# Optimization experiments

Measured on AMD Instinct MI355X. Metric: run time of the kernel, lower is better.

Reference implementation:

```python
import jax, jax.numpy as jnp
import numpy as np

N, E = 100000, 1600000
IN_C, HID_C, OUT_C = 128, 64, 40


def setup_inputs() -> dict:
    key = jax.random.key(0)
    ks = jax.random.split(key, 8)
    s = lambda fan_in: 1.0 / np.sqrt(fan_in)
    return {
        "x": jax.random.normal(ks[0], (N, IN_C), dtype=jnp.float32),
        "edge_index": jax.random.randint(ks[1], (2, E), 0, N, dtype=jnp.int64),
        # SAGEConv layer 1: lin_l (on aggregated neighbors, with bias) + lin_r (root, no bias)
        "W_l1": jax.random.uniform(ks[2], (IN_C, HID_C), jnp.float32, -s(IN_C), s(IN_C)),
        "b_l1": jnp.zeros((HID_C,), jnp.float32),
        "W_r1": jax.random.uniform(ks[3], (IN_C, HID_C), jnp.float32, -s(IN_C), s(IN_C)),
        # SAGEConv layer 2
        "W_l2": jax.random.uniform(ks[4], (HID_C, OUT_C), jnp.float32, -s(HID_C), s(HID_C)),
        "b_l2": jnp.zeros((OUT_C,), jnp.float32),
        "W_r2": jax.random.uniform(ks[5], (HID_C, OUT_C), jnp.float32, -s(HID_C), s(HID_C)),
    }


def _sage_conv(x, src, dst, W_l, b_l, W_r, n_nodes):
    # mean-aggregate neighbor features: scatter-add x[src] onto dst, divide by degree
    agg = jax.ops.segment_sum(x[src], dst, num_segments=n_nodes)  # [N, F]
    deg = jax.ops.segment_sum(jnp.ones((src.shape[0],), x.dtype), dst, num_segments=n_nodes)
    mean = agg / jnp.maximum(deg, 1.0)[:, None]
    return mean @ W_l + b_l + x @ W_r


def reference(x, edge_index, W_l1, b_l1, W_r1, W_l2, b_l2, W_r2):
    src, dst = edge_index[0], edge_index[1]  # messages flow src -> dst
    # eval mode: dropout is identity
    hid = _sage_conv(x, src, dst, W_l1, b_l1, W_r1, N)
    hid = jax.nn.relu(hid)
    out = _sage_conv(hid, src, dst, W_l2, b_l2, W_r2, N)
    return jax.nn.log_softmax(out, axis=1)
```

## Files before the change

### kernel.cpp

```cpp
#include <hip/hip_runtime.h>
#include <hip/hip_bf16.h>

#define N_NODES 100000
#define E_EDGES 1600000
#define IN_C 128
#define HID_C 64
#define OUT_C 40

#define NBUCK 196
#define BCAP 9216
#define B1_EPT 16
#define B1_CHUNK (256 * B1_EPT)
#define B1_GRID ((E_EDGES + B1_CHUNK - 1) / B1_CHUNK)

typedef unsigned short ushort_t;
typedef unsigned int uint_t;
typedef unsigned char uchar_t;
typedef __attribute__((ext_vector_type(8))) short bf16x8;
typedef __attribute__((ext_vector_type(4))) float f32x4;
typedef __attribute__((ext_vector_type(2))) float f32x2;

__device__ __forceinline__ float bfu2f(ushort_t u) {
    return __uint_as_float(((uint_t)u) << 16);
}
__device__ __forceinline__ ushort_t f2bfu(float f) {
    uint_t u = __float_as_uint(f);
    return (ushort_t)((u + 0x7FFFu + ((u >> 16) & 1u)) >> 16);
}
__device__ __forceinline__ uchar_t f2fp8(float f) {
    int p = __builtin_amdgcn_cvt_pk_fp8_f32(f, f, 0, false);
    return (uchar_t)(p & 0xff);
}
__device__ __forceinline__ float fp8_1(int u) {
    f32x2 f = __builtin_amdgcn_cvt_pk_f32_fp8(u, false);
    return f.x;
}

__global__ __launch_bounds__(256) void k_bucket(const int* __restrict__ src, const int* __restrict__ dst,
                                                int* __restrict__ bcur, int* __restrict__ bucket) {
    __shared__ int cnt[NBUCK];
    __shared__ int base[NBUCK];
    const int t = threadIdx.x;
    const int e0 = blockIdx.x * B1_CHUNK;

    for (int i = t; i < NBUCK; i += 256) cnt[i] = 0;
    __syncthreads();

    int myp[B1_EPT];
    int myb[B1_EPT];
#pragma unroll
    for (int j = 0; j < B1_EPT; ++j) {
        int e = e0 + t + j * 256;
        if (e < E_EDGES) {
            int d = dst[e];
            myp[j] = src[e] | ((d & 511) << 17);
            myb[j] = d >> 9;
            atomicAdd(&cnt[myb[j]], 1);
        } else {
            myb[j] = -1;
        }
    }
    __syncthreads();
    for (int i = t; i < NBUCK; i += 256) {
        base[i] = atomicAdd(&bcur[i], cnt[i]);
        cnt[i] = 0;
    }
    __syncthreads();
#pragma unroll
    for (int j = 0; j < B1_EPT; ++j) {
        if (myb[j] >= 0) {
            int b = myb[j];
            int loc = atomicAdd(&cnt[b], 1);
            int pos = base[b] + loc;
            if (pos < BCAP) bucket[(size_t)b * BCAP + pos] = myp[j];
        }
    }
}

__global__ __launch_bounds__(256) void k_scanS(const int* __restrict__ bcur, int* __restrict__ bbase,
                                               int* __restrict__ rowptr) {
    __shared__ int tmp[256];
    int t = threadIdx.x;
    int v = (t < NBUCK) ? min(bcur[t], BCAP) : 0;
    tmp[t] = v;
    __syncthreads();
    for (int off = 1; off < 256; off <<= 1) {
        int a = (t >= off) ? tmp[t - off] : 0;
        __syncthreads();
        tmp[t] += a;
        __syncthreads();
    }
    if (t < NBUCK) bbase[t] = tmp[t] - v;
    if (t == 0) rowptr[N_NODES] = tmp[255];
}

__global__ __launch_bounds__(256) void k_csr(const int* __restrict__ bucket, const int* __restrict__ bcur,
                                             const int* __restrict__ bbase,
                                             int* __restrict__ rowptr, int* __restrict__ csr) {
    __shared__ int hist[512];
    __shared__ int sc[2][512];
    __shared__ int cur[512];
    __shared__ int csrbuf[BCAP];
    const int t = threadIdx.x;
    const int b = blockIdx.x;
    const int n0 = b << 9;
    const int nb = min(512, N_NODES - n0);
    const int sz = min(bcur[b], BCAP);
    const int cbase = bbase[b];
    const int* bdata = bucket + (size_t)b * BCAP;

    for (int i = t; i < 512; i += 256) hist[i] = 0;
    __syncthreads();
    for (int i = t; i < sz; i += 256) {
        int p = bdata[i];
        atomicAdd(&hist[p >> 17], 1);
    }
    __syncthreads();
    for (int i = t; i < 512; i += 256) sc[0][i] = hist[i];
    __syncthreads();
    int pp = 0;
    for (int off = 1; off < 512; off <<= 1) {
        for (int i = t; i < 512; i += 256)
            sc[1 - pp][i] = sc[pp][i] + ((i >= off) ? sc[pp][i - off] : 0);
        __syncthreads();
        pp ^= 1;
    }
    for (int i = t; i < 512; i += 256) {
        int exc = sc[pp][i] - hist[i];
        cur[i] = exc;
        if (i < nb) rowptr[n0 + i] = cbase + exc;
    }
    __syncthreads();
    for (int i = t; i < sz; i += 256) {
        int p = bdata[i];
        int pos = atomicAdd(&cur[p >> 17], 1);
        csrbuf[pos] = p & 0x1FFFF;
    }
    __syncthreads();
    for (int i = t; i < sz; i += 256)
        csr[cbase + i] = csrbuf[i];
}

__global__ __launch_bounds__(256) void k_wprep(const float* __restrict__ Wl1, const float* __restrict__ Wr1,
                                               const float* __restrict__ Wl2, const float* __restrict__ Wr2,
                                               ushort_t* __restrict__ Wt1, ushort_t* __restrict__ Wt2) {
    int i = blockIdx.x * 256 + threadIdx.x;
    if (i < 128 * 128) {
        int n = i >> 7, k = i & 127;
        float v = (n < 64) ? Wl1[k * 64 + n] : Wr1[k * 64 + (n - 64)];
        Wt1[n * 128 + k] = f2bfu(v);
    }
    if (i < 80 * 64) {
        int n = i >> 6, k = i & 63;
        float v = (n < 40) ? Wl2[k * 40 + n] : Wr2[k * 40 + (n - 40)];
        Wt2[n * 64 + k] = f2bfu(v);
    }
}

__global__ __launch_bounds__(256) void k_gemm1(const float* __restrict__ x,
                                               const ushort_t* __restrict__ Wt,
                                               uchar_t* __restrict__ h1l,
                                               float* __restrict__ h1r) {
    __shared__ ushort_t xs[64 * 136];
    __shared__ ushort_t wsm[128 * 136];
    const int t = threadIdx.x;
    const int row_base = blockIdx.x * 64;

    for (int i = t; i < 128 * 16; i += 256) {
        int n = i >> 4, seg = i & 15;
        uint4 v = *(const uint4*)(Wt + n * 128 + seg * 8);
        *(uint4*)(wsm + n * 136 + seg * 8) = v;
    }
    for (int i = t; i < 64 * 32; i += 256) {
        int row = i >> 5, seg = i & 31;
        int gr = row_base + row;
        float4 v = make_float4(0.f, 0.f, 0.f, 0.f);
        if (gr < N_NODES) v = *(const float4*)(x + (size_t)gr * IN_C + seg * 4);
        ushort4 u;
        u.x = f2bfu(v.x); u.y = f2bfu(v.y); u.z = f2bfu(v.z); u.w = f2bfu(v.w);
        *(ushort4*)(xs + row * 136 + seg * 4) = u;
    }
    __syncthreads();

    const int wv = t >> 6, lane = t & 63;
    const int m = lane & 15, quad = lane >> 4;
    const int m0 = wv * 16;

    bf16x8 a[4];
#pragma unroll
    for (int kk = 0; kk < 4; ++kk)
        a[kk] = *(const bf16x8*)(xs + (m0 + m) * 136 + kk * 32 + quad * 8);

    f32x4 acc[8];
#pragma unroll
    for (int nt = 0; nt < 8; ++nt) acc[nt] = (f32x4){0.f, 0.f, 0.f, 0.f};

#pragma unroll
    for (int nt = 0; nt < 8; ++nt) {
#pragma unroll
        for (int kk = 0; kk < 4; ++kk) {
            bf16x8 b = *(const bf16x8*)(wsm + (nt * 16 + m) * 136 + kk * 32 + quad * 8);
            acc[nt] = __builtin_amdgcn_mfma_f32_16x16x32_bf16(a[kk], b, acc[nt], 0, 0, 0);
        }
    }

    const int grow_base = row_base + m0 + quad * 4;
#pragma unroll
    for (int r = 0; r < 4; ++r) {
        int grow = grow_base + r;
        if (grow < N_NODES) {
#pragma unroll
            for (int nt = 0; nt < 4; ++nt)
                h1l[(size_t)grow * HID_C + nt * 16 + m] = f2fp8(acc[nt][r]);
#pragma unroll
            for (int nt = 4; nt < 8; ++nt)
                h1r[(size_t)grow * HID_C + (nt - 4) * 16 + m] = acc[nt][r];
        }
    }
}

__global__ __launch_bounds__(256) void k_agg1(const int* __restrict__ rowptr, const int* __restrict__ csr,
                                              const uchar_t* __restrict__ h1l, const float* __restrict__ h1r,
                                              const float* __restrict__ b1, ushort_t* __restrict__ hid) {
    int row = (blockIdx.x * 256 + threadIdx.x) >> 6;
    int lane = threadIdx.x & 63;
    if (row >= N_NODES) return;
    int start = rowptr[row];
    int end = rowptr[row + 1];
    const uchar_t* colp = h1l + lane;
    float acc = 0.0f;
    int e = start;
    for (; e + 8 <= end; e += 8) {
        int s0 = csr[e],     s1 = csr[e + 1], s2 = csr[e + 2], s3 = csr[e + 3];
        int s4 = csr[e + 4], s5 = csr[e + 5], s6 = csr[e + 6], s7 = csr[e + 7];
        float v0 = fp8_1(colp[(size_t)s0 << 6]);
        float v1 = fp8_1(colp[(size_t)s1 << 6]);
        float v2 = fp8_1(colp[(size_t)s2 << 6]);
        float v3 = fp8_1(colp[(size_t)s3 << 6]);
        float v4 = fp8_1(colp[(size_t)s4 << 6]);
        float v5 = fp8_1(colp[(size_t)s5 << 6]);
        float v6 = fp8_1(colp[(size_t)s6 << 6]);
        float v7 = fp8_1(colp[(size_t)s7 << 6]);
        acc += ((v0 + v1) + (v2 + v3)) + ((v4 + v5) + (v6 + v7));
    }
    for (; e < end; ++e)
        acc += fp8_1(colp[(size_t)csr[e] << 6]);

    float inv = __builtin_amdgcn_rcpf(fmaxf((float)(end - start), 1.0f));
    float h = fmaxf(acc * inv + h1r[(size_t)row * HID_C + lane] + b1[lane], 0.0f);
    hid[(size_t)row * HID_C + lane] = f2bfu(h);
}

__global__ __launch_bounds__(256) void k_gemm2(const ushort_t* __restrict__ hid,
                                               const ushort_t* __restrict__ Wt,
                                               uchar_t* __restrict__ h2l,
                                               float* __restrict__ h2r) {
    __shared__ ushort_t hs[64 * 72];
    __shared__ ushort_t wsm[80 * 72];
    const int t = threadIdx.x;
    const int row_base = blockIdx.x * 64;

    for (int i = t; i < 80 * 8; i += 256) {
        int n = i >> 3, seg = i & 7;
        uint4 v = *(const uint4*)(Wt + n * 64 + seg * 8);
        *(uint4*)(wsm + n * 72 + seg * 8) = v;
    }
    for (int i = t; i < 64 * 8; i += 256) {
        int row = i >> 3, seg = i & 7;
        int gr = row_base + row;
        uint4 v = make_uint4(0u, 0u, 0u, 0u);
        if (gr < N_NODES) v = *(const uint4*)(hid + (size_t)gr * HID_C + seg * 8);
        *(uint4*)(hs + row * 72 + seg * 8) = v;
    }
    __syncthreads();

    const int wv = t >> 6, lane = t & 63;
    const int m = lane & 15, quad = lane >> 4;
    const int m0 = wv * 16;

    bf16x8 a[2];
#pragma unroll
    for (int kk = 0; kk < 2; ++kk)
        a[kk] = *(const bf16x8*)(hs + (m0 + m) * 72 + kk * 32 + quad * 8);

    f32x4 acc[5];
#pragma unroll
    for (int nt = 0; nt < 5; ++nt) acc[nt] = (f32x4){0.f, 0.f, 0.f, 0.f};

#pragma unroll
    for (int nt = 0; nt < 5; ++nt) {
#pragma unroll
        for (int kk = 0; kk < 2; ++kk) {
            bf16x8 b = *(const bf16x8*)(wsm + (nt * 16 + m) * 72 + kk * 32 + quad * 8);
            acc[nt] = __builtin_amdgcn_mfma_f32_16x16x32_bf16(a[kk], b, acc[nt], 0, 0, 0);
        }
    }

    const int grow_base = row_base + m0 + quad * 4;
#pragma unroll
    for (int r = 0; r < 4; ++r) {
        int grow = grow_base + r;
        if (grow < N_NODES) {
#pragma unroll
            for (int nt = 0; nt < 5; ++nt) {
                int col = nt * 16 + m;
                float v = acc[nt][r];
                if (col < OUT_C) h2l[(size_t)grow * 64 + col] = f2fp8(v);
                else             h2r[(size_t)grow * OUT_C + (col - OUT_C)] = v;
            }
        }
    }
}

__global__ __launch_bounds__(256) void k_agg2(const int* __restrict__ rowptr, const int* __restrict__ csr,
                                              const uchar_t* __restrict__ h2l, const float* __restrict__ h2r,
                                              const float* __restrict__ b2, float* __restrict__ out) {
    int row = (blockIdx.x * 256 + threadIdx.x) >> 6;
    int lane = threadIdx.x & 63;
    if (row >= N_NODES) return;
    int start = rowptr[row];
    int end = rowptr[row + 1];
    const uchar_t* colp = h2l + lane;
    float acc = 0.0f;
    int e = start;
    for (; e + 8 <= end; e += 8) {
        int s0 = csr[e],     s1 = csr[e + 1], s2 = csr[e + 2], s3 = csr[e + 3];
        int s4 = csr[e + 4], s5 = csr[e + 5], s6 = csr[e + 6], s7 = csr[e + 7];
        float v0 = fp8_1(colp[(size_t)s0 << 6]);
        float v1 = fp8_1(colp[(size_t)s1 << 6]);
        float v2 = fp8_1(colp[(size_t)s2 << 6]);
        float v3 = fp8_1(colp[(size_t)s3 << 6]);
        float v4 = fp8_1(colp[(size_t)s4 << 6]);
        float v5 = fp8_1(colp[(size_t)s5 << 6]);
        float v6 = fp8_1(colp[(size_t)s6 << 6]);
        float v7 = fp8_1(colp[(size_t)s7 << 6]);
        acc += ((v0 + v1) + (v2 + v3)) + ((v4 + v5) + (v6 + v7));
    }
    for (; e < end; ++e)
        acc += fp8_1(colp[(size_t)csr[e] << 6]);

    float inv = __builtin_amdgcn_rcpf(fmaxf((float)(end - start), 1.0f));
    float v = -1e30f;
    if (lane < OUT_C)
        v = acc * inv + h2r[(size_t)row * OUT_C + lane] + b2[lane];
    float m = v;
#pragma unroll
    for (int off = 1; off <= 32; off <<= 1)
        m = fmaxf(m, __shfl_xor(m, off));
    float ex = expf(v - m);
    float s = ex;
#pragma unroll
    for (int off = 1; off <= 32; off <<= 1)
        s += __shfl_xor(s, off);
    float res = v - m - logf(s);
    if (lane < OUT_C)
        out[(size_t)row * OUT_C + lane] = res;
}

extern "C" void kernel_launch(void* const* d_in, const int* in_sizes, int n_in,
                              void* d_out, int out_size, void* d_ws, size_t ws_size,
                              hipStream_t stream) {
    const float* x   = (const float*)d_in[0];
    const int*   ei  = (const int*)d_in[1];
    const float* Wl1 = (const float*)d_in[2];
    const float* b1  = (const float*)d_in[3];
    const float* Wr1 = (const float*)d_in[4];
    const float* Wl2 = (const float*)d_in[5];
    const float* b2  = (const float*)d_in[6];
    const float* Wr2 = (const float*)d_in[7];

    size_t u = 0;
    int*      bucket = (int*)d_ws;             u += (size_t)NBUCK * BCAP;
    int*      bcur   = (int*)d_ws + u;         u += NBUCK;
    int*      bbase  = (int*)d_ws + u;         u += NBUCK + 4;
    int*      rowptr = (int*)d_ws + u;         u += N_NODES + 1;
    int*      csr    = (int*)d_ws + u;         u += E_EDGES;
    u = (u + 3) & ~(size_t)3;
    ushort_t* Wt1    = (ushort_t*)((int*)d_ws + u); u += 128 * 128 / 2;
    ushort_t* Wt2    = (ushort_t*)((int*)d_ws + u); u += 80 * 64 / 2;
    uchar_t*  h1l    = (uchar_t*)((int*)d_ws + u);  u += (size_t)N_NODES * HID_C / 4;
    float*    h1r    = (float*)d_ws + u;       u += (size_t)N_NODES * HID_C;
    ushort_t* hid    = (ushort_t*)((int*)d_ws + u); u += (size_t)N_NODES * HID_C / 2;
    uchar_t*  h2l    = (uchar_t*)((int*)d_ws + u);  u += (size_t)N_NODES * 64 / 4;
    float*    h2r    = (float*)d_ws + u;       u += (size_t)N_NODES * OUT_C;
    if (ws_size < u * 4) return;

    hipMemsetAsync(bcur, 0, NBUCK * sizeof(int), stream);

    const int* src = ei;
    const int* dst = ei + E_EDGES;

    k_wprep<<<64, 256, 0, stream>>>(Wl1, Wr1, Wl2, Wr2, Wt1, Wt2);
    k_bucket<<<B1_GRID, 256, 0, stream>>>(src, dst, bcur, bucket);
    k_scanS<<<1, 256, 0, stream>>>(bcur, bbase, rowptr);
    k_csr<<<NBUCK, 256, 0, stream>>>(bucket, bcur, bbase, rowptr, csr);

    k_gemm1<<<(N_NODES + 63) / 64, 256, 0, stream>>>(x, Wt1, h1l, h1r);
    k_agg1<<<N_NODES / 4, 256, 0, stream>>>(rowptr, csr, h1l, h1r, b1, hid);
    k_gemm2<<<(N_NODES + 63) / 64, 256, 0, stream>>>(hid, Wt2, h2l, h2r);
    k_agg2<<<N_NODES / 4, 256, 0, stream>>>(rowptr, csr, h2l, h2r, b2, (float*)d_out);
}
```

Before: 309.4 us.

## Gather 8 edges per wave with 8-byte fp8 vector loads in aggregation kernels

Both aggregation kernels now split each 64-lane wave into 8 edge slots of 8 lanes. Each lane loads 8 fp8 features as one uint2 and accumulates them into 8 registers, followed by a cross-slot shuffle reduction. The epilogues use vectorized float4 loads and stores, and the log-softmax reduces over 8 lanes instead of 64. This replaces the old per-lane single-byte gathers to cut load instruction count, at the cost of extra shuffles and idle lanes in layer 2, where only 5 of the 8 parts are valid.

```diff
diff --git a/kernel.cpp b/kernel.cpp
--- a/kernel.cpp
+++ b/kernel.cpp
@@ -30,10 +30,6 @@
 __device__ __forceinline__ uchar_t f2fp8(float f) {
     int p = __builtin_amdgcn_cvt_pk_fp8_f32(f, f, 0, false);
     return (uchar_t)(p & 0xff);
-}
-__device__ __forceinline__ float fp8_1(int u) {
-    f32x2 f = __builtin_amdgcn_cvt_pk_f32_fp8(u, false);
-    return f.x;
 }
 
 __global__ __launch_bounds__(256) void k_bucket(const int* __restrict__ src, const int* __restrict__ dst,
@@ -227,28 +223,46 @@
     if (row >= N_NODES) return;
     int start = rowptr[row];
     int end = rowptr[row + 1];
-    const uchar_t* colp = h1l + lane;
-    float acc = 0.0f;
-    int e = start;
-    for (; e + 8 <= end; e += 8) {
-        int s0 = csr[e],     s1 = csr[e + 1], s2 = csr[e + 2], s3 = csr[e + 3];
-        int s4 = csr[e + 4], s5 = csr[e + 5], s6 = csr[e + 6], s7 = csr[e + 7];
-        float v0 = fp8_1(colp[(size_t)s0 << 6]);
-        float v1 = fp8_1(colp[(size_t)s1 << 6]);
-        float v2 = fp8_1(colp[(size_t)s2 << 6]);
-        float v3 = fp8_1(colp[(size_t)s3 << 6]);
-        float v4 = fp8_1(colp[(size_t)s4 << 6]);
-        float v5 = fp8_1(colp[(size_t)s5 << 6]);
-        float v6 = fp8_1(colp[(size_t)s6 << 6]);
-        float v7 = fp8_1(colp[(size_t)s7 << 6]);
-        acc += ((v0 + v1) + (v2 + v3)) + ((v4 + v5) + (v6 + v7));
-    }
-    for (; e < end; ++e)
-        acc += fp8_1(colp[(size_t)csr[e] << 6]);
-
-    float inv = __builtin_amdgcn_rcpf(fmaxf((float)(end - start), 1.0f));
-    float h = fmaxf(acc * inv + h1r[(size_t)row * HID_C + lane] + b1[lane], 0.0f);
-    hid[(size_t)row * HID_C + lane] = f2bfu(h);
+    const int slot = lane >> 3;
+    const int part = lane & 7;
+    float acc[8] = {0.f, 0.f, 0.f, 0.f, 0.f, 0.f, 0.f, 0.f};
+
+    for (int base = start; base < end; base += 8) {
+        int e = base + slot;
+        int ee = min(e, end - 1);
+        int s = csr[ee];
+        uint2 u = *(const uint2*)(h1l + ((size_t)s << 6) + part * 8);
+        if (e >= end) { u.x = 0u; u.y = 0u; }
+        f32x2 f;
+        f = __builtin_amdgcn_cvt_pk_f32_fp8(u.x, false); acc[0] += f.x; acc[1] += f.y;
+        f = __builtin_amdgcn_cvt_pk_f32_fp8(u.x, true);  acc[2] += f.x; acc[3] += f.y;
+        f = __builtin_amdgcn_cvt_pk_f32_fp8(u.y, false); acc[4] += f.x; acc[5] += f.y;
+        f = __builtin_amdgcn_cvt_pk_f32_fp8(u.y, true);  acc[6] += f.x; acc[7] += f.y;
+    }
+#pragma unroll
+    for (int off = 8; off <= 32; off <<= 1)
+#pragma unroll
+        for (int j = 0; j < 8; ++j)
+            acc[j] += __shfl_xor(acc[j], off);
+
+    if (slot == 0) {
+        float inv = __builtin_amdgcn_rcpf(fmaxf((float)(end - start), 1.0f));
+        size_t bi = (size_t)row * HID_C + part * 8;
+        float4 r0 = *(const float4*)(h1r + bi);
+        float4 r1 = *(const float4*)(h1r + bi + 4);
+        float4 bb0 = *(const float4*)(b1 + part * 8);
+        float4 bb1 = *(const float4*)(b1 + part * 8 + 4);
+        ushort_t o[8];
+        o[0] = f2bfu(fmaxf(acc[0] * inv + r0.x + bb0.x, 0.f));
+        o[1] = f2bfu(fmaxf(acc[1] * inv + r0.y + bb0.y, 0.f));
+        o[2] = f2bfu(fmaxf(acc[2] * inv + r0.z + bb0.z, 0.f));
+        o[3] = f2bfu(fmaxf(acc[3] * inv + r0.w + bb0.w, 0.f));
+        o[4] = f2bfu(fmaxf(acc[4] * inv + r1.x + bb1.x, 0.f));
+        o[5] = f2bfu(fmaxf(acc[5] * inv + r1.y + bb1.y, 0.f));
+        o[6] = f2bfu(fmaxf(acc[6] * inv + r1.z + bb1.z, 0.f));
+        o[7] = f2bfu(fmaxf(acc[7] * inv + r1.w + bb1.w, 0.f));
+        *(uint4*)(hid + bi) = *(const uint4*)o;
+    }
 }
 
 __global__ __launch_bounds__(256) void k_gemm2(const ushort_t* __restrict__ hid,
@@ -320,41 +334,66 @@
     if (row >= N_NODES) return;
     int start = rowptr[row];
     int end = rowptr[row + 1];
-    const uchar_t* colp = h2l + lane;
-    float acc = 0.0f;
-    int e = start;
-    for (; e + 8 <= end; e += 8) {
-        int s0 = csr[e],     s1 = csr[e + 1], s2 = csr[e + 2], s3 = csr[e + 3];
-        int s4 = csr[e + 4], s5 = csr[e + 5], s6 = csr[e + 6], s7 = csr[e + 7];
-        float v0 = fp8_1(colp[(size_t)s0 << 6]);
-        float v1 = fp8_1(colp[(size_t)s1 << 6]);
-        float v2 = fp8_1(colp[(size_t)s2 << 6]);
-        float v3 = fp8_1(colp[(size_t)s3 << 6]);
-        float v4 = fp8_1(colp[(size_t)s4 << 6]);
-        float v5 = fp8_1(colp[(size_t)s5 << 6]);
-        float v6 = fp8_1(colp[(size_t)s6 << 6]);
-        float v7 = fp8_1(colp[(size_t)s7 << 6]);
-        acc += ((v0 + v1) + (v2 + v3)) + ((v4 + v5) + (v6 + v7));
-    }
-    for (; e < end; ++e)
-        acc += fp8_1(colp[(size_t)csr[e] << 6]);
-
+    const int slot = lane >> 3;
+    const int part = lane & 7;
+    const bool pvalid = part < 5;
+    float acc[8] = {0.f, 0.f, 0.f, 0.f, 0.f, 0.f, 0.f, 0.f};
+
+    for (int base = start; base < end; base += 8) {
+        int e = base + slot;
+        int ee = min(e, end - 1);
+        int s = csr[ee];
+        uint2 u = *(const uint2*)(h2l + ((size_t)s << 6) + part * 8);
+        if (e >= end || !pvalid) { u.x = 0u; u.y = 0u; }
+        f32x2 f;
+        f = __builtin_amdgcn_cvt_pk_f32_fp8(u.x, false); acc[0] += f.x; acc[1] += f.y;
+        f = __builtin_amdgcn_cvt_pk_f32_fp8(u.x, true);  acc[2] += f.x; acc[3] += f.y;
+        f = __builtin_amdgcn_cvt_pk_f32_fp8(u.y, false); acc[4] += f.x; acc[5] += f.y;
+        f = __builtin_amdgcn_cvt_pk_f32_fp8(u.y, true);  acc[6] += f.x; acc[7] += f.y;
+    }
+#pragma unroll
+    for (int off = 8; off <= 32; off <<= 1)
+#pragma unroll
+        for (int j = 0; j < 8; ++j)
+            acc[j] += __shfl_xor(acc[j], off);
+
+    const bool fin = (slot == 0) && pvalid;
     float inv = __builtin_amdgcn_rcpf(fmaxf((float)(end - start), 1.0f));
-    float v = -1e30f;
-    if (lane < OUT_C)
-        v = acc * inv + h2r[(size_t)row * OUT_C + lane] + b2[lane];
-    float m = v;
-#pragma unroll
-    for (int off = 1; off <= 32; off <<= 1)
-        m = fmaxf(m, __shfl_xor(m, off));
-    float ex = expf(v - m);
-    float s = ex;
-#pragma unroll
-    for (int off = 1; off <= 32; off <<= 1)
-        s += __shfl_xor(s, off);
-    float res = v - m - logf(s);
-    if (lane < OUT_C)
-        out[(size_t)row * OUT_C + lane] = res;
+    float v[8];
+    if (fin) {
+        size_t bi = (size_t)row * OUT_C + part * 8;
+        float4 r0 = *(const float4*)(h2r + bi);
+        float4 r1 = *(const float4*)(h2r + bi + 4);
+        float4 bb0 = *(const float4*)(b2 + part * 8);
+        float4 bb1 = *(const float4*)(b2 + part * 8 + 4);
+        v[0] = acc[0] * inv + r0.x + bb0.x;
+        v[1] = acc[1] * inv + r0.y + bb0.y;
+        v[2] = acc[2] * inv + r0.z + bb0.z;
+        v[3] = acc[3] * inv + r0.w + bb0.w;
+        v[4] = acc[4] * inv + r1.x + bb1.x;
+        v[5] = acc[5] * inv + r1.y + bb1.y;
+        v[6] = acc[6] * inv + r1.z + bb1.z;
+        v[7] = acc[7] * inv + r1.w + bb1.w;
+    } else {
+#pragma unroll
+        for (int j = 0; j < 8; ++j) v[j] = -1e30f;
+    }
+    float pm = v[0];
+#pragma unroll
+    for (int j = 1; j < 8; ++j) pm = fmaxf(pm, v[j]);
+#pragma unroll
+    for (int off = 1; off <= 4; off <<= 1) pm = fmaxf(pm, __shfl_xor(pm, off));
+    float es = 0.f;
+#pragma unroll
+    for (int j = 0; j < 8; ++j) es += expf(v[j] - pm);
+#pragma unroll
+    for (int off = 1; off <= 4; off <<= 1) es += __shfl_xor(es, off);
+    float ls = logf(es);
+    if (fin) {
+        size_t bo = (size_t)row * OUT_C + part * 8;
+        *(float4*)(out + bo) = make_float4(v[0] - pm - ls, v[1] - pm - ls, v[2] - pm - ls, v[3] - pm - ls);
+        *(float4*)(out + bo + 4) = make_float4(v[4] - pm - ls, v[5] - pm - ls, v[6] - pm - ls, v[7] - pm - ls);
+    }
 }
 
 extern "C" void kernel_launch(void* const* d_in, const int* in_sizes, int n_in,
```

Result: faster. 277.1 us (-10.5%).
